# Kernel optimization log

Measured on AMD Instinct MI355X. Metric: run time of the kernel, lower is better.

The kernel has to match this reference:

```python
import jax, jax.numpy as jnp
import numpy as np

DIM = 512
DIM2 = 2 * DIM
HEADS = 8
HEAD_DIM = DIM2 // HEADS
NB = 4                      # BlockDiagonalLinear blocks
BLK = DIM2 // NB
KS = 4                      # causal conv kernel size
EPS = 1e-5


def setup_inputs() -> dict:
    key = jax.random.key(0)
    ks = jax.random.split(key, 32)
    r = lambda i, shape, s=0.02: jax.random.normal(ks[i], shape, dtype=jnp.float32) * s
    inp = {
        "x": jax.random.normal(ks[0], (2, 2048, DIM), dtype=jnp.float32),
        "ln_w": jnp.ones((DIM,), jnp.float32),
        "ln_b": jnp.zeros((DIM,), jnp.float32),
        "mlp1_w": r(1, (DIM, DIM2)), "mlp1_b": jnp.zeros((DIM2,), jnp.float32),
        "mlp2_w": r(2, (DIM, DIM2)), "mlp2_b": jnp.zeros((DIM2,), jnp.float32),
        "conv_w": r(3, (DIM2, DIM2, KS)), "conv_b": jnp.zeros((DIM2,), jnp.float32),
        "bq_w": r(4, (NB, BLK, BLK)), "bk_w": r(5, (NB, BLK, BLK)), "bv_w": r(6, (NB, BLK, BLK)),
        "wq_w": r(7, (DIM2, DIM2)), "wq_b": jnp.zeros((DIM2,), jnp.float32),
        "wk_w": r(8, (DIM2, DIM2)), "wk_b": jnp.zeros((DIM2,), jnp.float32),
        "wv_w": r(9, (DIM2, DIM2)), "wv_b": jnp.zeros((DIM2,), jnp.float32),
        "wi_w": r(10, (DIM2, HEADS)), "wi_b": jnp.zeros((HEADS,), jnp.float32),
        "wf_w": r(11, (DIM2, HEADS)), "wf_b": jnp.zeros((HEADS,), jnp.float32),
        "gn_w": jnp.ones((DIM2,), jnp.float32), "gn_b": jnp.zeros((DIM2,), jnp.float32),
        "skip": jnp.ones((DIM2,), jnp.float32),
        "fin_w": r(12, (DIM2, DIM)), "fin_b": jnp.zeros((DIM,), jnp.float32),
    }
    return inp


def _layernorm(x, w, b):
    mu = jnp.mean(x, -1, keepdims=True)
    var = jnp.var(x, -1, keepdims=True)
    return (x - mu) * jax.lax.rsqrt(var + EPS) * w + b


def _block_linear(x, w):  # x: [b,s,DIM2], w: [NB, BLK, BLK]
    b, s, _ = x.shape
    xg = x.reshape(b, s, NB, BLK)
    return jnp.einsum('bsgi,gio->bsgo', xg, w).reshape(b, s, DIM2)


def _mlstm_cell(q, k, v, wq_w, wq_b, wk_w, wk_b, wv_w, wv_b,
                wi_w, wi_b, wf_w, wf_b, gn_w, gn_b):
    b, s, _ = q.shape
    tau = DIM2 ** 0.5
    itilde = jnp.einsum('bsd,dh->bhs', q, wi_w) + wi_b[None, :, None]   # [b,h,s]
    ftilde = jnp.einsum('bsd,dh->bhs', k, wf_w) + wf_b[None, :, None]   # [b,h,s]
    # cumulative log forget gates; F_act[i,j] = cs[i] - cs[j] on lower triangle
    cs = jnp.cumsum(jax.nn.log_sigmoid(ftilde), axis=-1)                # [b,h,s]
    mask = jnp.tril(jnp.ones((s, s), bool))
    Dtilde = jnp.where(mask,
                       cs[..., :, None] - cs[..., None, :] + itilde[..., None, :],
                       -jnp.inf)                                        # [b,h,s,s]
    max_d = jnp.max(Dtilde, axis=-1, keepdims=True)
    D = jnp.exp(Dtilde - max_d)
    qh = (q @ wq_w + wq_b).reshape(b, s, HEADS, HEAD_DIM).transpose(0, 2, 1, 3)
    kh = (k @ wk_w + wk_b).reshape(b, s, HEADS, HEAD_DIM).transpose(0, 2, 1, 3)
    vh = (v @ wv_w + wv_b).reshape(b, s, HEADS, HEAD_DIM).transpose(0, 2, 1, 3)
    Ctilde = jnp.einsum('bhid,bhjd->bhij', qh, kh) * D / tau
    maxit = jnp.maximum(jnp.abs(Ctilde.sum(-1)), jnp.exp(-max_d[..., 0]))  # [b,h,s]
    H = jnp.einsum('bhij,bhjd->bhid', Ctilde, vh) / (maxit[..., None] + 1e-8)
    H = H.transpose(0, 2, 1, 3)                                          # [b,s,h,hd]
    # GroupNorm(heads, DIM2): per (b,s,head-group) normalization
    mu = jnp.mean(H, -1, keepdims=True)
    var = jnp.var(H, -1, keepdims=True)
    Hn = (H - mu) * jax.lax.rsqrt(var + EPS)
    Hn = Hn * gn_w.reshape(HEADS, HEAD_DIM) + gn_b.reshape(HEADS, HEAD_DIM)
    return Hn.reshape(b, s, DIM2)


def reference(x, ln_w, ln_b, mlp1_w, mlp1_b, mlp2_w, mlp2_b, conv_w, conv_b,
              bq_w, bk_w, bv_w, wq_w, wq_b, wk_w, wk_b, wv_w, wv_b,
              wi_w, wi_b, wf_w, wf_b, gn_w, gn_b, skip, fin_w, fin_b):
    inputs = _layernorm(x, ln_w, ln_b)
    a = inputs @ mlp1_w + mlp1_b                 # [b,s,DIM2]
    bgate = jax.nn.silu(inputs @ mlp2_w + mlp2_b)
    # causal conv1d (left pad KS-1)
    ac = a.transpose(0, 2, 1)                    # [b,DIM2,s]
    qk = jax.lax.conv_general_dilated(ac, conv_w, (1,), [(KS - 1, 0)],
                                      dimension_numbers=('NCH', 'OIH', 'NCH'))
    qk = (qk + conv_b[None, :, None]).transpose(0, 2, 1)
    qk = jax.nn.silu(qk)
    q = _block_linear(qk, bq_w)
    k = _block_linear(qk, bk_w)
    v = _block_linear(a, bv_w)
    out1 = _mlstm_cell(q, k, v, wq_w, wq_b, wk_w, wk_b, wv_w, wv_b,
                       wi_w, wi_b, wf_w, wf_b, gn_w, gn_b)
    out1 = out1 + skip * qk
    out1 = out1 * bgate
    out1 = out1 @ fin_w + fin_b
    return x + out1
```

## Files before the change

kernel.cpp:

```cpp
#include <hip/hip_runtime.h>
#include <hip/hip_bf16.h>
#include <cmath>

typedef __hip_bfloat16 bf16;
typedef __attribute__((ext_vector_type(8))) short short8;
typedef __attribute__((ext_vector_type(4))) float f32x4;

#define SEQ   2048
#define DIMX  512
#define DIM2X 1024
#define NHEADS 8
#define HDIM  128
#define EPSF  1e-5f
#define PADROWS 2051

__device__ __forceinline__ float b2f(bf16 v) { return __bfloat162float(v); }
__device__ __forceinline__ bf16 f2b(float f) { return __float2bfloat16(f); }
__device__ __forceinline__ unsigned short f2bu(float f) { bf16 t = __float2bfloat16(f); return *(unsigned short*)&t; }

__device__ __forceinline__ void gl16(const bf16* g, bf16* l) {
  __builtin_amdgcn_global_load_lds((const __attribute__((address_space(1))) void*)g,
                                   (__attribute__((address_space(3))) void*)l, 16, 0, 0);
}

__global__ void __launch_bounds__(256) k_layernorm(const float* __restrict__ x,
                                                   const float* __restrict__ w,
                                                   const float* __restrict__ b,
                                                   bf16* __restrict__ out) {
  int row  = blockIdx.x * 4 + (threadIdx.x >> 6);
  int lane = threadIdx.x & 63;
  const float* xr = x + (size_t)row * DIMX;
  float v[8]; float s = 0.f, sq = 0.f;
#pragma unroll
  for (int i = 0; i < 8; i++) {
    float f = xr[lane + i * 64];
    v[i] = f; s += f; sq += f * f;
  }
#pragma unroll
  for (int off = 32; off; off >>= 1) { s += __shfl_xor(s, off); sq += __shfl_xor(sq, off); }
  float mu  = s * (1.f / DIMX);
  float var = sq * (1.f / DIMX) - mu * mu;
  float rs  = rsqrtf(var + EPSF);
  bf16* o = out + (size_t)row * DIMX;
#pragma unroll
  for (int i = 0; i < 8; i++) {
    int c = lane + i * 64;
    o[c] = f2b((v[i] - mu) * rs * w[c] + b[c]);
  }
}

__global__ void __launch_bounds__(256) k_castT3(const float* __restrict__ W0,
                                                const float* __restrict__ W1,
                                                const float* __restrict__ W2,
                                                bf16* __restrict__ WT,
                                                int K, int N, int innerZ, int gW, int gT) {
  __shared__ float t[32][33];
  const int z = blockIdx.z;
  const int sel = z / innerZ, zz = z % innerZ;
  const float* W = (sel == 0 ? W0 : sel == 1 ? W1 : W2) + (size_t)zz * gW;
  bf16* T = WT + (size_t)(sel * innerZ + zz) * gT;
  const int k0 = blockIdx.y * 32, n0 = blockIdx.x * 32;
  const int r = threadIdx.x >> 5, c = threadIdx.x & 31;
#pragma unroll
  for (int i = 0; i < 4; i++)
    t[r + i * 8][c] = W[(size_t)(k0 + r + i * 8) * N + n0 + c];
  __syncthreads();
#pragma unroll
  for (int i = 0; i < 4; i++)
    T[(size_t)(n0 + r + i * 8) * K + k0 + c] = f2b(t[c][r + i * 8]);
}

__global__ void __launch_bounds__(256) k_convwT(const float* __restrict__ cw, bf16* __restrict__ wc) {
  int idx = blockIdx.x * 256 + threadIdx.x;
  int o = idx >> 12, z = idx & 4095, kk = z >> 10, i = z & 1023;
  wc[idx] = f2b(cw[(size_t)o * 4096 + i * 4 + kk]);
}

__global__ void __launch_bounds__(256) k_zeropad(bf16* __restrict__ p) {
  int idx = blockIdx.x * 256 + threadIdx.x;
  int b = idx / 3072, off = idx % 3072;
  p[(size_t)b * PADROWS * DIM2X + off] = f2b(0.f);
}

__device__ __forceinline__ void mgemm_body(const bf16* A, int lda, const bf16* WT,
                                           const float* bias, void* Cv, const float* xres,
                                           int ldc, int K, int ACT, int STORE, int APAD,
                                           size_t coff, int bm, int bn) {
  __shared__ __align__(16) bf16 smA[4][128 * 32];
  __shared__ __align__(16) bf16 smB[4][64 * 32];
  const int tid  = threadIdx.x;
  const int lane = tid & 63;
  const int w = tid >> 6, wy = w >> 1, wx = w & 1;
  const int col = lane & 15, quad = lane >> 4;

  const int r4 = tid >> 2, c8 = (tid & 3) * 8;
  int ra0 = bm + r4, ra1 = bm + 64 + r4;
  if (APAD) { ra0 += (ra0 >> 11) * 3 + 3; ra1 += (ra1 >> 11) * 3 + 3; }
  const bf16* gA0 = A + (size_t)ra0 * lda + c8;
  const bf16* gA1 = A + (size_t)ra1 * lda + c8;
  const bf16* gB0 = WT + (size_t)(bn + r4) * K + c8;

  f32x4 acc[4][2];
#pragma unroll
  for (int a = 0; a < 4; a++)
#pragma unroll
    for (int b = 0; b < 2; b++) acc[a][b] = (f32x4){0.f, 0.f, 0.f, 0.f};

  const int laoff = (wy * 64) * 32, lboff = (wx * 32) * 32;
  const int lsa = r4 * 32 + c8;
  const int nsteps = K >> 5;

#define GSTAGE(buf, k0s)                                                       \
  do {                                                                         \
    gl16(gA0 + (k0s), &smA[buf][lsa]);                                         \
    gl16(gA1 + (k0s), &smA[buf][64 * 32 + lsa]);                               \
    gl16(gB0 + (k0s), &smB[buf][lsa]);                                         \
  } while (0)

  GSTAGE(0, 0);
  if (nsteps > 1) GSTAGE(1, 32);
  for (int s = 0; s < nsteps; ++s) {
    if (s + 2 < nsteps) GSTAGE((s + 2) & 3, (s + 2) * 32);
    if (s + 2 < nsteps)      asm volatile("s_waitcnt vmcnt(6)" ::: "memory");
    else if (s + 1 < nsteps) asm volatile("s_waitcnt vmcnt(3)" ::: "memory");
    else                     asm volatile("s_waitcnt vmcnt(0)" ::: "memory");
    __builtin_amdgcn_s_barrier();
    asm volatile("" ::: "memory");
    const bf16* bA = smA[s & 3];
    const bf16* bB = smB[s & 3];
    short8 af[4], bfr[2];
#pragma unroll
    for (int mt = 0; mt < 4; mt++)
      af[mt] = *(const short8*)&bA[laoff + (mt * 16 + col) * 32 + quad * 8];
#pragma unroll
    for (int nt = 0; nt < 2; nt++)
      bfr[nt] = *(const short8*)&bB[lboff + (nt * 16 + col) * 32 + quad * 8];
#pragma unroll
    for (int mt = 0; mt < 4; mt++)
#pragma unroll
      for (int nt = 0; nt < 2; nt++)
        acc[mt][nt] = __builtin_amdgcn_mfma_f32_16x16x32_bf16(af[mt], bfr[nt], acc[mt][nt], 0, 0, 0);
  }
#undef GSTAGE

#pragma unroll
  for (int mt = 0; mt < 4; mt++) {
#pragma unroll
    for (int nt = 0; nt < 2; nt++) {
      const int n = bn + wx * 32 + nt * 16 + col;
      const int mrow0 = bm + wy * 64 + mt * 16 + quad * 4;
      float bs = bias ? bias[n] : 0.f;
      if (STORE == 1) {
        bf16* C = (bf16*)Cv + coff;
        ushort4 pk;
        pk.x = f2bu(acc[mt][nt][0] + bs); pk.y = f2bu(acc[mt][nt][1] + bs);
        pk.z = f2bu(acc[mt][nt][2] + bs); pk.w = f2bu(acc[mt][nt][3] + bs);
        *(ushort4*)(C + (size_t)n * 4096 + mrow0) = pk;
      } else if (STORE == 2) {
        float* O = (float*)Cv + coff;
#pragma unroll
        for (int r = 0; r < 4; r++) {
          size_t gi = (size_t)(mrow0 + r) * ldc + n;
          O[gi] = acc[mt][nt][r] + bs + xres[gi];
        }
      } else if (STORE == 3) {
        bf16* C = (bf16*)Cv;
        const int pr = (mrow0 >> 11) * 3 + 3;
#pragma unroll
        for (int r = 0; r < 4; r++)
          C[(size_t)(mrow0 + pr + r) * ldc + n] = f2b(acc[mt][nt][r] + bs);
      } else {
        bf16* C = (bf16*)Cv + coff;
#pragma unroll
        for (int r = 0; r < 4; r++) {
          float v = acc[mt][nt][r] + bs;
          if (ACT == 1) v = v / (1.f + expf(-v));
          C[(size_t)(mrow0 + r) * ldc + n] = f2b(v);
        }
      }
    }
  }
}

__device__ __forceinline__ int xcd_work_id() {
  const int nx = gridDim.x, ny = gridDim.y;
  const int d = blockIdx.x + nx * (blockIdx.y + ny * blockIdx.z);
  const int q = (nx * ny * (int)gridDim.z) >> 3;
  return (d & 7) * q + (d >> 3);
}

template <int ACT, int STORE, int APAD>
__global__ void __launch_bounds__(256) k_mgemm(const bf16* __restrict__ A, int lda,
                                               const bf16* __restrict__ WT,
                                               const float* __restrict__ bias,
                                               void* __restrict__ Cv,
                                               const float* __restrict__ xres,
                                               int ldc, int K,
                                               int gA, int gW, int gC) {
  const int wk = xcd_work_id();
  const int nx = gridDim.x, ny = gridDim.y;
  const int wx = wk % nx, rest = wk / nx;
  const int wy = rest % ny, g = rest / ny;
  mgemm_body(A + (size_t)g * gA, lda, WT + (size_t)g * gW, bias, Cv, xres,
             ldc, K, ACT, STORE, APAD, (size_t)g * gC, wy * 128, wx * 64);
}

__global__ void __launch_bounds__(256) k_mgemmB(const bf16* A0, const bf16* A1, const bf16* A2,
                                                const bf16* W0, const bf16* W1, const bf16* W2,
                                                const float* b0, const float* b1, const float* b2,
                                                void* C0, void* C1, void* C2,
                                                int lda, int ldc, int K, int zPer,
                                                int gA, int gW, int gC,
                                                int actm, int storem, int apadm) {
  const int wk = xcd_work_id();
  const int nx = gridDim.x, ny = gridDim.y;
  const int wx = wk % nx, rest = wk / nx;
  const int wy = rest % ny, z = rest / ny;
  const int sel = z / zPer, zz = z % zPer;
  const bf16* A = (sel == 0 ? A0 : sel == 1 ? A1 : A2) + (size_t)zz * gA;
  const bf16* W = (sel == 0 ? W0 : sel == 1 ? W1 : W2) + (size_t)zz * gW;
  const float* bias = sel == 0 ? b0 : sel == 1 ? b1 : b2;
  void* Cv = sel == 0 ? C0 : sel == 1 ? C1 : C2;
  mgemm_body(A, lda, W, bias, Cv, nullptr, ldc, K,
             (actm >> sel) & 1, (storem >> (4 * sel)) & 15, (apadm >> sel) & 1,
             (size_t)zz * gC, wy * 128, wx * 64);
}

__global__ void __launch_bounds__(256) k_gates(const bf16* __restrict__ q, const bf16* __restrict__ kk,
                                               const float* __restrict__ wi, const float* __restrict__ wib,
                                               const float* __restrict__ wf, const float* __restrict__ wfb,
                                               float* __restrict__ it, float* __restrict__ ft) {
  int gid  = blockIdx.x * 4 + (threadIdx.x >> 6);
  int lane = threadIdx.x & 63;
  int which = gid >> 12;
  int m = gid & 4095;
  const bf16* row = (which ? kk : q) + (size_t)m * DIM2X;
  const float* w = which ? wf : wi;
  float s[8] = {0, 0, 0, 0, 0, 0, 0, 0};
  for (int d = lane; d < DIM2X; d += 64) {
    float xv = b2f(row[d]);
    const float4* wp = (const float4*)(w + d * 8);
    float4 w0 = wp[0], w1 = wp[1];
    s[0] += xv * w0.x; s[1] += xv * w0.y; s[2] += xv * w0.z; s[3] += xv * w0.w;
    s[4] += xv * w1.x; s[5] += xv * w1.y; s[6] += xv * w1.z; s[7] += xv * w1.w;
  }
#pragma unroll
  for (int off = 32; off; off >>= 1) {
#pragma unroll
    for (int h = 0; h < 8; h++) s[h] += __shfl_xor(s[h], off);
  }
  if (lane == 0) {
    int b_ = m >> 11, tt = m & 2047;
    const float* wb = which ? wfb : wib;
    float* dst = which ? ft : it;
#pragma unroll
    for (int h = 0; h < 8; h++)
      dst[((size_t)(b_ * NHEADS + h)) * SEQ + tt] = s[h] + wb[h];
  }
}

__global__ void __launch_bounds__(256) k_scan(const float* __restrict__ it, const float* __restrict__ ft,
                                              float* __restrict__ cs, float* __restrict__ md) {
  const int bh = blockIdx.x;
  const int t  = threadIdx.x;
  const float* fr = ft + (size_t)bh * SEQ;
  const float* ir = it + (size_t)bh * SEQ;
  float* csr = cs + (size_t)bh * SEQ;
  float* mdr = md + (size_t)bh * SEQ;
  __shared__ float tmp[256];
  float loc[8]; float run = 0.f;
#pragma unroll
  for (int j = 0; j < 8; j++) {
    float xv = fr[t * 8 + j];
    float ls = fminf(xv, 0.f) - log1pf(expf(-fabsf(xv)));
    run += ls; loc[j] = run;
  }
  tmp[t] = run;
  __syncthreads();
  for (int off = 1; off < 256; off <<= 1) {
    float add = (t >= off) ? tmp[t - off] : 0.f;
    __syncthreads();
    tmp[t] += add;
    __syncthreads();
  }
  float exc = (t == 0) ? 0.f : tmp[t - 1];
  float csv[8];
#pragma unroll
  for (int j = 0; j < 8; j++) { csv[j] = loc[j] + exc; csr[t * 8 + j] = csv[j]; }
  __syncthreads();
  float rmax = -INFINITY; float gm[8];
#pragma unroll
  for (int j = 0; j < 8; j++) {
    float gv = ir[t * 8 + j] - csv[j];
    rmax = fmaxf(rmax, gv); gm[j] = rmax;
  }
  tmp[t] = rmax;
  __syncthreads();
  for (int off = 1; off < 256; off <<= 1) {
    float other = (t >= off) ? tmp[t - off] : -INFINITY;
    __syncthreads();
    tmp[t] = fmaxf(tmp[t], other);
    __syncthreads();
  }
  float emax = (t == 0) ? -INFINITY : tmp[t - 1];
#pragma unroll
  for (int j = 0; j < 8; j++) mdr[t * 8 + j] = csv[j] + fmaxf(gm[j], emax);
}

__global__ void __launch_bounds__(256) k_attn_mfma(const bf16* __restrict__ qh,
                                                   const bf16* __restrict__ kh,
                                                   const bf16* __restrict__ vt,
                                                   const float* __restrict__ cs,
                                                   const float* __restrict__ md,
                                                   const float* __restrict__ itl,
                                                   const bf16* __restrict__ qk,
                                                   const bf16* __restrict__ bg,
                                                   const float* __restrict__ gw,
                                                   const float* __restrict__ gb,
                                                   const float* __restrict__ skip,
                                                   bf16* __restrict__ pre) {
  const int bh = blockIdx.y, b_ = bh >> 3, h = bh & 7;
  const int bx = blockIdx.x;
  const int tile = ((blockIdx.y >> 3) & 1) ? bx : 31 - bx;
  const int i0 = tile * 64;
  const int tid = threadIdx.x;
  const int w = tid >> 6;
  const int lane = tid & 63;
  const int col = lane & 15, quad = lane >> 4;
  const int i0w = i0 + w * 16;
  const int iwmax = i0w + 15;
  const float L2E = 1.44269504f;

  __shared__ __align__(16) bf16 smK[4 * 4096];
  __shared__ __align__(16) bf16 smV[4 * 4096];
  __shared__ __align__(16) bf16 Sc[4][16][40];

  const size_t baseQK = ((size_t)b_ * SEQ) * DIM2X + (size_t)h * HDIM;
  const size_t vtb = (size_t)(h * HDIM) * 4096 + (size_t)b_ * SEQ;
  const float* csp = cs + (size_t)bh * SEQ;
  const float* mdp = md + (size_t)bh * SEQ;
  const float* itp = itl + (size_t)bh * SEQ;

  short8 qf[4];
#pragma unroll
  for (int kc = 0; kc < 4; kc++)
    qf[kc] = *(const short8*)(qh + baseQK + (size_t)(i0w + col) * DIM2X + kc * 32 + quad * 8);

  float cs_i[4], md_i[4];
#pragma unroll
  for (int r = 0; r < 4; r++) {
    int i = i0w + quad * 4 + r;
    cs_i[r] = csp[i] * L2E; md_i[r] = mdp[i] * L2E;
  }

  f32x4 accpv[8];
#pragma unroll
  for (int nb = 0; nb < 8; nb++) accpv[nb] = (f32x4){0.f, 0.f, 0.f, 0.f};
  float rs[4] = {0.f, 0.f, 0.f, 0.f};

  const int kj = tid >> 4, kq = tid & 15;
  const bf16* gKs = kh + baseQK + (size_t)kj * DIM2X + ((kq ^ (kj & 7)) * 8);
  const int vn = tid >> 2, vq = tid & 3;
  const bf16* gVs = vt + vtb + (size_t)vn * 4096 + ((vq ^ ((vn >> 1) & 3)) * 8);

  const int trips = 2 * tile + 2;

#define STAGE(buf, j0s)                                                        \
  do {                                                                         \
    bf16* dK = &smK[(buf) * 4096 + tid * 8];                                   \
    gl16(gKs + (size_t)(j0s) * DIM2X, dK);                                     \
    gl16(gKs + (size_t)((j0s) + 16) * DIM2X, dK + 2048);                       \
    bf16* dV = &smV[(buf) * 4096 + tid * 8];                                   \
    gl16(gVs + (j0s), dV);                                                     \
    gl16(gVs + (j0s) + (size_t)64 * 4096, dV + 2048);                          \
  } while (0)

  STAGE(0, 0);
  STAGE(1, 32);
  for (int t = 0; t < trips; ++t) {
    const int cur = t & 3;
    const int j0p = t * 32;
    if (t + 2 < trips) STAGE((t + 2) & 3, j0p + 64);
    if (t + 2 < trips)      asm volatile("s_waitcnt vmcnt(8)" ::: "memory");
    else if (t + 1 < trips) asm volatile("s_waitcnt vmcnt(4)" ::: "memory");
    else                    asm volatile("s_waitcnt vmcnt(0)" ::: "memory");
    __builtin_amdgcn_s_barrier();
    asm volatile("" ::: "memory");
    if (j0p <= iwmax) {
      float g0 = (itp[j0p + col] - csp[j0p + col]) * L2E;
      float g1 = (itp[j0p + 16 + col] - csp[j0p + 16 + col]) * L2E;
      const bool jt1 = (j0p + 16 <= iwmax);
#pragma unroll
      for (int jt = 0; jt < 2; jt++) {
        const int j0 = j0p + jt * 16;
        float sv[4] = {0.f, 0.f, 0.f, 0.f};
        if (jt == 0 || jt1) {
          const int jj = jt * 16 + col;
          f32x4 aq = (f32x4){0.f, 0.f, 0.f, 0.f};
#pragma unroll
          for (int kc = 0; kc < 4; kc++) {
            short8 bk = *(const short8*)&smK[cur * 4096 + jj * 128 + ((((kc << 2) | quad) ^ (jj & 7)) << 3)];
            aq = __builtin_amdgcn_mfma_f32_16x16x32_bf16(qf[kc], bk, aq, 0, 0, 0);
          }
          const int j = j0 + col;
          const float gj = jt ? g1 : g0;
#pragma unroll
          for (int r = 0; r < 4; r++) {
            const int i = i0w + quad * 4 + r;
            float s = (j <= i) ? exp2f(cs_i[r] + gj - md_i[r] - 5.f) * aq[r] : 0.f;
            sv[r] = s; rs[r] += s;
          }
        }
#pragma unroll
        for (int r = 0; r < 4; r++) Sc[w][quad * 4 + r][jt * 16 + col] = f2b(sv[r]);
      }
      asm volatile("s_waitcnt lgkmcnt(0)" ::: "memory");
      __builtin_amdgcn_sched_barrier(0);
      short8 af = *(const short8*)(&Sc[w][col][quad * 8]);
#pragma unroll
      for (int nb = 0; nb < 8; nb++) {
        const int rn = nb * 16 + col;
        short8 bv = *(const short8*)&smV[cur * 4096 + rn * 32 + ((quad ^ ((rn >> 1) & 3)) << 3)];
        accpv[nb] = __builtin_amdgcn_mfma_f32_16x16x32_bf16(af, bv, accpv[nb], 0, 0, 0);
      }
    }
  }
#undef STAGE

#pragma unroll
  for (int r = 0; r < 4; r++) {
    float v = rs[r];
    v += __shfl_xor(v, 1); v += __shfl_xor(v, 2);
    v += __shfl_xor(v, 4); v += __shfl_xor(v, 8);
    rs[r] = v;
  }
  float inv[4];
#pragma unroll
  for (int r = 0; r < 4; r++) {
    float maxit = fmaxf(fabsf(rs[r]), exp2f(fminf(-md_i[r], 43.f)));
    inv[r] = 1.f / (maxit + 1e-8f);
  }
  float gwv[8], gbv[8], skv[8];
#pragma unroll
  for (int nb = 0; nb < 8; nb++) {
    int c = h * HDIM + nb * 16 + col;
    gwv[nb] = gw[c]; gbv[nb] = gb[c]; skv[nb] = skip[c];
  }
#pragma unroll
  for (int r = 0; r < 4; r++) {
    const int row = i0w + quad * 4 + r;
    float s1 = 0.f, s2 = 0.f;
#pragma unroll
    for (int nb = 0; nb < 8; nb++) {
      float v = accpv[nb][r] * inv[r];
      s1 += v; s2 += v * v;
    }
    s1 += __shfl_xor(s1, 1); s2 += __shfl_xor(s2, 1);
    s1 += __shfl_xor(s1, 2); s2 += __shfl_xor(s2, 2);
    s1 += __shfl_xor(s1, 4); s2 += __shfl_xor(s2, 4);
    s1 += __shfl_xor(s1, 8); s2 += __shfl_xor(s2, 8);
    float mu  = s1 * (1.f / 128.f);
    float var = s2 * (1.f / 128.f) - mu * mu;
    float rsg = rsqrtf(var + EPSF);
    const size_t rbase = baseQK + (size_t)row * DIM2X;
#pragma unroll
    for (int nb = 0; nb < 8; nb++) {
      float hv = accpv[nb][r] * inv[r];
      float hn = (hv - mu) * rsg * gwv[nb] + gbv[nb];
      size_t gi = rbase + nb * 16 + col;
      pre[gi] = f2b((hn + skv[nb] * b2f(qk[gi])) * b2f(bg[gi]));
    }
  }
}

extern "C" void kernel_launch(void* const* d_in, const int* in_sizes, int n_in,
                              void* d_out, int out_size, void* d_ws, size_t ws_size,
                              hipStream_t stream) {
  const float* x     = (const float*)d_in[0];
  const float* ln_w  = (const float*)d_in[1];
  const float* ln_b  = (const float*)d_in[2];
  const float* mlp1w = (const float*)d_in[3];
  const float* mlp1b = (const float*)d_in[4];
  const float* mlp2w = (const float*)d_in[5];
  const float* mlp2b = (const float*)d_in[6];
  const float* convw = (const float*)d_in[7];
  const float* convb = (const float*)d_in[8];
  const float* bqw   = (const float*)d_in[9];
  const float* bkw   = (const float*)d_in[10];
  const float* bvw   = (const float*)d_in[11];
  const float* wqw   = (const float*)d_in[12];
  const float* wqb   = (const float*)d_in[13];
  const float* wkw   = (const float*)d_in[14];
  const float* wkb   = (const float*)d_in[15];
  const float* wvw   = (const float*)d_in[16];
  const float* wvb   = (const float*)d_in[17];
  const float* wiw   = (const float*)d_in[18];
  const float* wib   = (const float*)d_in[19];
  const float* wfw   = (const float*)d_in[20];
  const float* wfb   = (const float*)d_in[21];
  const float* gnw   = (const float*)d_in[22];
  const float* gnb   = (const float*)d_in[23];
  const float* skip  = (const float*)d_in[24];
  const float* finw  = (const float*)d_in[25];
  const float* finb  = (const float*)d_in[26];
  float* out = (float*)d_out;

  float* GA  = (float*)d_ws;
  float* ITb = GA;
  float* FTb = GA + 32768;
  float* CSb = GA + 65536;
  float* MDb = GA + 98304;
  const size_t SLOT = 4u * 1024u * 1024u;
  bf16* S0 = (bf16*)((char*)d_ws + (1 << 20));
  bf16* S1 = S0 + SLOT;
  bf16* S2 = S1 + SLOT;
  bf16* S3 = S2 + SLOT;
  bf16* S4 = S3 + SLOT;
  bf16* S5 = S4 + SLOT;
  bf16* S6 = S5 + SLOT;
  bf16 *LN = S0, *BG = S2, *QKb = S3, *Qb = S4, *Kb = S5, *Vb = S6;
  bf16 *QH = S0, *KH = S1, *VT = S4, *PRE = S6;
  bf16* WTb   = S6 + SLOT;
  bf16* mlp1T = WTb;
  bf16* mlp2T = WTb + 524288;
  bf16* convT = WTb + 1048576;
  bf16* bqT   = WTb + 5242880;
  bf16* bkT   = bqT + 262144;
  bf16* bvT   = bkT + 262144;
  bf16* wqT   = bvT + 262144;
  bf16* wkT   = wqT + 1048576;
  bf16* wvT   = wkT + 1048576;
  bf16* finT  = wvT + 1048576;
  bf16* APD   = finT + 524288;

  k_castT3<<<dim3(32, 16, 2), 256, 0, stream>>>(mlp1w, mlp2w, mlp2w, mlp1T, DIMX, DIM2X, 1, 0, 524288);
  k_castT3<<<dim3(32, 32, 3), 256, 0, stream>>>(wqw, wkw, wvw, wqT, DIM2X, DIM2X, 1, 0, 1048576);
  k_castT3<<<dim3(8, 8, 12), 256, 0, stream>>>(bqw, bkw, bvw, bqT, 256, 256, 4, 65536, 65536);
  k_castT3<<<dim3(16, 32, 1), 256, 0, stream>>>(finw, finw, finw, finT, DIM2X, DIMX, 1, 0, 524288);
  k_convwT<<<16384, 256, 0, stream>>>(convw, convT);
  k_zeropad<<<24, 256, 0, stream>>>(APD);

  k_layernorm<<<1024, 256, 0, stream>>>(x, ln_w, ln_b, LN);
  k_mgemmB<<<dim3(16, 32, 2), 256, 0, stream>>>(LN, LN, LN, mlp1T, mlp2T, mlp2T,
                                                mlp1b, mlp2b, mlp2b, APD, BG, BG,
                                                DIMX, DIM2X, DIMX, 1, 0, 0, 0,
                                                 0b10,  3 | (0 << 4),  0);
  k_mgemm<1, 0, 0><<<dim3(16, 16, 2), 256, 0, stream>>>(APD, DIM2X, convT, convb, QKb, nullptr,
                                                        DIM2X, 4096, PADROWS * DIM2X, 0, SEQ * DIM2X);
  k_mgemmB<<<dim3(4, 32, 12), 256, 0, stream>>>(QKb, QKb, APD, bqT, bkT, bvT,
                                                nullptr, nullptr, nullptr, Qb, Kb, Vb,
                                                DIM2X, DIM2X, 256, 4, 256, 65536, 256,
                                                 0,  0,  0b100);
  k_gates<<<2048, 256, 0, stream>>>(Qb, Kb, wiw, wib, wfw, wfb, ITb, FTb);
  k_scan<<<16, 256, 0, stream>>>(ITb, FTb, CSb, MDb);
  k_mgemmB<<<dim3(16, 32, 3), 256, 0, stream>>>(Qb, Kb, Vb, wqT, wkT, wvT,
                                                wqb, wkb, wvb, QH, KH, VT,
                                                DIM2X, DIM2X, DIM2X, 1, 0, 0, 0,
                                                 0,  0 | (0 << 4) | (1 << 8),  0);
  k_attn_mfma<<<dim3(32, 16), 256, 0, stream>>>(QH, KH, VT, CSb, MDb, ITb,
                                                QKb, BG, gnw, gnb, skip, PRE);
  k_mgemm<0, 2, 0><<<dim3(8, 32), 256, 0, stream>>>(PRE, DIM2X, finT, finb, out, x, DIMX, DIM2X, 0, 0, 0);
}
```

Baseline: 444.9 us.

## Deepen GEMM K-tile to 64 with XOR-swizzled LDS and triple buffering

The shared GEMM body now loads 64-wide K tiles into three LDS buffers instead of 32-wide tiles into four. An XOR swizzle on the 16-byte chunks is meant to avoid LDS bank conflicts on the MFMA fragment reads, and the next prefetch is issued after the barrier so the buffer being overwritten is no longer in use. Larger tiles halve the barrier count per GEMM but raise LDS use per block, which may reduce occupancy. Separately, the conv weight transpose now reads float4 and writes four strided outputs per thread, using a quarter as many threads.

```diff
diff --git a/kernel.cpp b/kernel.cpp
--- a/kernel.cpp
+++ b/kernel.cpp
@@ -72,8 +72,13 @@
 
 __global__ void __launch_bounds__(256) k_convwT(const float* __restrict__ cw, bf16* __restrict__ wc) {
   int idx = blockIdx.x * 256 + threadIdx.x;
-  int o = idx >> 12, z = idx & 4095, kk = z >> 10, i = z & 1023;
-  wc[idx] = f2b(cw[(size_t)o * 4096 + i * 4 + kk]);
+  int o = idx >> 10, i = idx & 1023;
+  float4 v = *(const float4*)(cw + (size_t)idx * 4);
+  size_t base = (size_t)o * 4096 + i;
+  wc[base]        = f2b(v.x);
+  wc[base + 1024] = f2b(v.y);
+  wc[base + 2048] = f2b(v.z);
+  wc[base + 3072] = f2b(v.w);
 }
 
 __global__ void __launch_bounds__(256) k_zeropad(bf16* __restrict__ p) {
@@ -86,19 +91,26 @@
                                            const float* bias, void* Cv, const float* xres,
                                            int ldc, int K, int ACT, int STORE, int APAD,
                                            size_t coff, int bm, int bn) {
-  __shared__ __align__(16) bf16 smA[4][128 * 32];
-  __shared__ __align__(16) bf16 smB[4][64 * 32];
+  __shared__ __align__(16) bf16 smA[3][128 * 64];
+  __shared__ __align__(16) bf16 smB[3][64 * 64];
   const int tid  = threadIdx.x;
   const int lane = tid & 63;
   const int w = tid >> 6, wy = w >> 1, wx = w & 1;
   const int col = lane & 15, quad = lane >> 4;
 
-  const int r4 = tid >> 2, c8 = (tid & 3) * 8;
-  int ra0 = bm + r4, ra1 = bm + 64 + r4;
-  if (APAD) { ra0 += (ra0 >> 11) * 3 + 3; ra1 += (ra1 >> 11) * 3 + 3; }
-  const bf16* gA0 = A + (size_t)ra0 * lda + c8;
-  const bf16* gA1 = A + (size_t)ra1 * lda + c8;
-  const bf16* gB0 = WT + (size_t)(bn + r4) * K + c8;
+  const int r8 = tid >> 3, c8i = tid & 7;
+  const int swz = (c8i ^ (r8 & 7)) * 8;
+  const bf16* gA[4];
+#pragma unroll
+  for (int p = 0; p < 4; p++) {
+    int ra = bm + r8 + p * 32;
+    if (APAD) ra += (ra >> 11) * 3 + 3;
+    gA[p] = A + (size_t)ra * lda + swz;
+  }
+  const bf16* gB[2];
+#pragma unroll
+  for (int p = 0; p < 2; p++)
+    gB[p] = WT + (size_t)(bn + r8 + p * 32) * K + swz;
 
   f32x4 acc[4][2];
 #pragma unroll
@@ -106,40 +118,54 @@
 #pragma unroll
     for (int b = 0; b < 2; b++) acc[a][b] = (f32x4){0.f, 0.f, 0.f, 0.f};
 
-  const int laoff = (wy * 64) * 32, lboff = (wx * 32) * 32;
-  const int lsa = r4 * 32 + c8;
-  const int nsteps = K >> 5;
+  const int nsteps = K >> 6;
 
 #define GSTAGE(buf, k0s)                                                       \
   do {                                                                         \
-    gl16(gA0 + (k0s), &smA[buf][lsa]);                                         \
-    gl16(gA1 + (k0s), &smA[buf][64 * 32 + lsa]);                               \
-    gl16(gB0 + (k0s), &smB[buf][lsa]);                                         \
+    bf16* dA = &smA[buf][tid * 8];                                             \
+    gl16(gA[0] + (k0s), dA);                                                   \
+    gl16(gA[1] + (k0s), dA + 2048);                                            \
+    gl16(gA[2] + (k0s), dA + 4096);                                            \
+    gl16(gA[3] + (k0s), dA + 6144);                                            \
+    bf16* dB = &smB[buf][tid * 8];                                             \
+    gl16(gB[0] + (k0s), dB);                                                   \
+    gl16(gB[1] + (k0s), dB + 2048);                                            \
   } while (0)
 
   GSTAGE(0, 0);
-  if (nsteps > 1) GSTAGE(1, 32);
+  GSTAGE(1, 64);
+  int buf = 0;
   for (int s = 0; s < nsteps; ++s) {
-    if (s + 2 < nsteps) GSTAGE((s + 2) & 3, (s + 2) * 32);
-    if (s + 2 < nsteps)      asm volatile("s_waitcnt vmcnt(6)" ::: "memory");
-    else if (s + 1 < nsteps) asm volatile("s_waitcnt vmcnt(3)" ::: "memory");
-    else                     asm volatile("s_waitcnt vmcnt(0)" ::: "memory");
+    if (s + 1 < nsteps) asm volatile("s_waitcnt vmcnt(6)" ::: "memory");
+    else                asm volatile("s_waitcnt vmcnt(0)" ::: "memory");
     __builtin_amdgcn_s_barrier();
+    if (s + 2 < nsteps) {
+      int nb = buf + 2; if (nb >= 3) nb -= 3;
+      GSTAGE(nb, (s + 2) * 64);
+    }
     asm volatile("" ::: "memory");
-    const bf16* bA = smA[s & 3];
-    const bf16* bB = smB[s & 3];
-    short8 af[4], bfr[2];
-#pragma unroll
-    for (int mt = 0; mt < 4; mt++)
-      af[mt] = *(const short8*)&bA[laoff + (mt * 16 + col) * 32 + quad * 8];
-#pragma unroll
-    for (int nt = 0; nt < 2; nt++)
-      bfr[nt] = *(const short8*)&bB[lboff + (nt * 16 + col) * 32 + quad * 8];
-#pragma unroll
-    for (int mt = 0; mt < 4; mt++)
-#pragma unroll
-      for (int nt = 0; nt < 2; nt++)
-        acc[mt][nt] = __builtin_amdgcn_mfma_f32_16x16x32_bf16(af[mt], bfr[nt], acc[mt][nt], 0, 0, 0);
+    const bf16* bA = smA[buf];
+    const bf16* bB = smB[buf];
+#pragma unroll
+    for (int kc = 0; kc < 2; kc++) {
+      short8 af[4], bfr[2];
+#pragma unroll
+      for (int mt = 0; mt < 4; mt++) {
+        const int row = wy * 64 + mt * 16 + col;
+        af[mt] = *(const short8*)&bA[row * 64 + (((kc * 4 + quad) ^ (row & 7)) << 3)];
+      }
+#pragma unroll
+      for (int nt = 0; nt < 2; nt++) {
+        const int row = wx * 32 + nt * 16 + col;
+        bfr[nt] = *(const short8*)&bB[row * 64 + (((kc * 4 + quad) ^ (row & 7)) << 3)];
+      }
+#pragma unroll
+      for (int mt = 0; mt < 4; mt++)
+#pragma unroll
+        for (int nt = 0; nt < 2; nt++)
+          acc[mt][nt] = __builtin_amdgcn_mfma_f32_16x16x32_bf16(af[mt], bfr[nt], acc[mt][nt], 0, 0, 0);
+    }
+    if (++buf >= 3) buf = 0;
   }
 #undef GSTAGE
 
@@ -537,7 +563,7 @@
   k_castT3<<<dim3(32, 32, 3), 256, 0, stream>>>(wqw, wkw, wvw, wqT, DIM2X, DIM2X, 1, 0, 1048576);
   k_castT3<<<dim3(8, 8, 12), 256, 0, stream>>>(bqw, bkw, bvw, bqT, 256, 256, 4, 65536, 65536);
   k_castT3<<<dim3(16, 32, 1), 256, 0, stream>>>(finw, finw, finw, finT, DIM2X, DIMX, 1, 0, 524288);
-  k_convwT<<<16384, 256, 0, stream>>>(convw, convT);
+  k_convwT<<<4096, 256, 0, stream>>>(convw, convT);
   k_zeropad<<<24, 256, 0, stream>>>(APD);
 
   k_layernorm<<<1024, 256, 0, stream>>>(x, ln_w, ln_b, LN);
```

Result: no change. 442.6 us (-0.5%).
